# Performance work log

Measured on AMD Instinct MI355X. Metric: run time of the kernel, lower is better.

Reference implementation:

```python
import jax, jax.numpy as jnp
import numpy as np

M_ZEROS = 15
ZETA_WEIGHT = 0.4
SIGMA = 0.1
# First 15 imaginary parts of nontrivial Riemann zeta zeros (get_zeta_zeros(15))
ZETA_ZEROS = np.array([
    14.134725, 21.022040, 25.010858, 30.424876, 32.935062,
    37.586178, 40.918719, 43.327073, 48.005151, 49.773832,
    52.970321, 56.446248, 59.347044, 60.831779, 65.112544,
], dtype=np.float32)

B, T, I, H = 64, 1024, 512, 512


def setup_inputs() -> dict:
    key = jax.random.key(0)
    k = jax.random.split(key, 6)
    s_ih = 1.0 / np.sqrt(I)
    s_hh = 1.0 / np.sqrt(H)
    x = jax.random.normal(k[0], (B, T, I), dtype=jnp.float32)
    W_ih = jax.random.normal(k[1], (4 * H, I), dtype=jnp.float32) * s_ih
    W_hh = jax.random.normal(k[2], (4 * H, H), dtype=jnp.float32) * s_hh
    b_ih = jax.random.normal(k[3], (4 * H,), dtype=jnp.float32) * s_hh
    b_hh = jax.random.normal(k[4], (4 * H,), dtype=jnp.float32) * s_hh
    gammas = jnp.asarray(ZETA_ZEROS)
    phi_init = np.exp(-SIGMA * np.abs(ZETA_ZEROS))
    log_phi = jnp.asarray(np.log(np.exp(phi_init) - 1 + 1e-6).astype(np.float32))
    return {"x": x, "W_ih": W_ih, "W_hh": W_hh, "b_ih": b_ih,
            "b_hh": b_hh, "log_phi": log_phi, "gammas": gammas}


def _zeta_lstm(x, W_ih, W_hh, b_ih, b_hh, log_phi, gammas):
    Bq, Tq, _ = x.shape
    Hq = W_hh.shape[1]
    # Precompute scalar zeta mixing weight per timestep: w_t = sum(phi * cos(g*t)) / M
    phi = jax.nn.softplus(log_phi)                     # [M]
    t_idx = jnp.arange(Tq, dtype=jnp.float32)          # [T]
    cos_mat = jnp.cos(t_idx[:, None] * gammas[None, :])  # [T, M]
    w_ts = (cos_mat @ phi) / M_ZEROS                   # [T]
    # Hoist the input projection out of the scan: [B,T,4H]
    x_proj = jnp.einsum('bti,gi->btg', x, W_ih) + b_ih + b_hh

    def step(carry, inp):
        h, c = carry
        xp_t, w_t = inp
        gates = xp_t + h @ W_hh.T                      # [B, 4H]
        ig, fg, gg, og = jnp.split(gates, 4, axis=-1)
        c_new = jax.nn.sigmoid(fg) * c + jax.nn.sigmoid(ig) * jnp.tanh(gg)
        h_new = jax.nn.sigmoid(og) * jnp.tanh(c_new)
        # zeta memory uses the PREVIOUS h
        h_out = h_new + ZETA_WEIGHT * (w_t * h)
        return (h_out, c_new), h_out

    h0 = jnp.zeros((Bq, Hq), dtype=x.dtype)
    c0 = jnp.zeros((Bq, Hq), dtype=x.dtype)
    xs = (jnp.transpose(x_proj, (1, 0, 2)), w_ts)
    (h_f, c_f), outs = jax.lax.scan(step, (h0, c0), xs)
    outputs = jnp.transpose(outs, (1, 0, 2))           # [B, T, H]
    return outputs, h_f[None, :, :], c_f[None, :, :]


def reference(x, W_ih, W_hh, b_ih, b_hh, log_phi, gammas):
    return _zeta_lstm(x, W_ih, W_hh, b_ih, b_hh, log_phi, gammas)
```

## Files before the change

kernel.cpp:

```cpp
#include <hip/hip_runtime.h>

#define BDIM 64
#define TDIM 1024
#define IDIM 512
#define HDIM 512
#define G4   2048
#define DSLAB 8
#define SLAB_ELEMS (BDIM * HDIM)
#define GROUP_ELEMS (16 * HDIM)

typedef unsigned short u16;
typedef unsigned int u32;
typedef unsigned long long u64;
typedef __attribute__((ext_vector_type(8))) short short8;
typedef __attribute__((ext_vector_type(4))) float f32x4;

__device__ __forceinline__ u16 f2bf(float f) {
    union { float f; unsigned u; } v; v.f = f;
    unsigned u = v.u;
    return (u16)((u + 0x7fffu + ((u >> 16) & 1u)) >> 16);
}
__device__ __forceinline__ float bf2f(u16 h) {
    union { unsigned u; float f; } v; v.u = ((unsigned)h) << 16;
    return v.f;
}
__device__ __forceinline__ float fsig(float x) {
    float e = __builtin_amdgcn_exp2f(x * -1.4426950408889634f);
    return __builtin_amdgcn_rcpf(1.0f + e);
}
__device__ __forceinline__ float ftanh(float x) {
    float e = __builtin_amdgcn_exp2f(x * -2.8853900817779268f);
    return 2.0f * __builtin_amdgcn_rcpf(1.0f + e) - 1.0f;
}

__global__ void prep_kernel(const float* __restrict__ Whh,
                            const float* __restrict__ bih,
                            const float* __restrict__ bhh,
                            const float* __restrict__ log_phi,
                            const float* __restrict__ gammas,
                            u16* __restrict__ whh_bf,
                            float* __restrict__ bias,
                            float* __restrict__ wfull,
                            u32* __restrict__ hbuf32) {
    int idx = blockIdx.x * 256 + threadIdx.x;
    if (idx < G4 * HDIM) whh_bf[idx] = f2bf(Whh[idx]);
    if (idx < G4) bias[idx] = bih[idx] + bhh[idx];
    if (idx < DSLAB * (SLAB_ELEMS / 2))
        hbuf32[idx] = (idx < (SLAB_ELEMS / 2)) ? 0u : 0xffffffffu;
    if (idx < TDIM) {
        float acc = 0.0f;
        #pragma unroll
        for (int m = 0; m < 15; ++m) {
            float lp = log_phi[m];
            float sp = (lp > 15.0f) ? lp : log1pf(expf(lp));
            acc += sp * cosf((float)idx * gammas[m]);
        }
        wfull[idx] = 0.4f * acc / 15.0f;
    }
}

__global__ __launch_bounds__(256) void xproj_gemm(
        const float* __restrict__ X, const float* __restrict__ Wih,
        const float* __restrict__ bias, u16* __restrict__ xproj) {
    const int tid  = threadIdx.x;
    const int m0   = blockIdx.x * 128;
    const int n0   = blockIdx.y * 128;
    const int lane = tid & 63, w = tid >> 6;
    const int l16  = lane & 15, lhi = lane >> 4;
    const int wr   = w >> 1, wc = w & 1;

    __shared__ u16 As[128 * 64];
    __shared__ u16 Bs[128 * 64];

    f32x4 acc[4][4];
    #pragma unroll
    for (int i = 0; i < 4; ++i)
        #pragma unroll
        for (int j = 0; j < 4; ++j) acc[i][j] = (f32x4){0.f, 0.f, 0.f, 0.f};

    for (int kt = 0; kt < 8; ++kt) {
        const int k0 = kt * 64;
        __syncthreads();
        #pragma unroll
        for (int p = 0; p < 4; ++p) {
            int g = p * 256 + tid;
            int row = g >> 3, oct = g & 7;
            const float* src = X + (size_t)(m0 + row) * IDIM + k0 + oct * 8;
            float4 v0 = *(const float4*)src;
            float4 v1 = *(const float4*)(src + 4);
            short8 u;
            u[0] = (short)f2bf(v0.x); u[1] = (short)f2bf(v0.y);
            u[2] = (short)f2bf(v0.z); u[3] = (short)f2bf(v0.w);
            u[4] = (short)f2bf(v1.x); u[5] = (short)f2bf(v1.y);
            u[6] = (short)f2bf(v1.z); u[7] = (short)f2bf(v1.w);
            int so = (oct ^ (row & 7)) * 8;
            *(short8*)&As[row * 64 + so] = u;
        }
        #pragma unroll
        for (int p = 0; p < 4; ++p) {
            int g = p * 256 + tid;
            int row = g >> 3, oct = g & 7;
            const float* src = Wih + (size_t)(n0 + row) * IDIM + k0 + oct * 8;
            float4 v0 = *(const float4*)src;
            float4 v1 = *(const float4*)(src + 4);
            short8 u;
            u[0] = (short)f2bf(v0.x); u[1] = (short)f2bf(v0.y);
            u[2] = (short)f2bf(v0.z); u[3] = (short)f2bf(v0.w);
            u[4] = (short)f2bf(v1.x); u[5] = (short)f2bf(v1.y);
            u[6] = (short)f2bf(v1.z); u[7] = (short)f2bf(v1.w);
            int so = (oct ^ (row & 7)) * 8;
            *(short8*)&Bs[row * 64 + so] = u;
        }
        __syncthreads();
        #pragma unroll
        for (int ks = 0; ks < 2; ++ks) {
            short8 a[4], b[4];
            #pragma unroll
            for (int ai = 0; ai < 4; ++ai) {
                int row = 64 * wr + 16 * ai + l16;
                int oct = (4 * ks + lhi) ^ (row & 7);
                a[ai] = *(const short8*)&As[row * 64 + oct * 8];
            }
            #pragma unroll
            for (int bi = 0; bi < 4; ++bi) {
                int row = 64 * wc + 16 * bi + l16;
                int oct = (4 * ks + lhi) ^ (row & 7);
                b[bi] = *(const short8*)&Bs[row * 64 + oct * 8];
            }
            #pragma unroll
            for (int ai = 0; ai < 4; ++ai)
                #pragma unroll
                for (int bi = 0; bi < 4; ++bi)
                    acc[ai][bi] = __builtin_amdgcn_mfma_f32_16x16x32_bf16(
                        a[ai], b[bi], acc[ai][bi], 0, 0, 0);
        }
    }
    float bv[4];
    #pragma unroll
    for (int bi = 0; bi < 4; ++bi) bv[bi] = bias[n0 + 64 * wc + 16 * bi + l16];
    #pragma unroll
    for (int ai = 0; ai < 4; ++ai) {
        int grow_base = m0 + 64 * wr + 16 * ai + 4 * lhi;
        #pragma unroll
        for (int bi = 0; bi < 4; ++bi) {
            int gcol = n0 + 64 * wc + 16 * bi + l16;
            #pragma unroll
            for (int r = 0; r < 4; ++r) {
                int grow = grow_base + r;
                int b = grow >> 10;
                int t = grow & 1023;
                xproj[((size_t)t * BDIM + b) * G4 + gcol] =
                    f2bf(acc[ai][bi][r] + bv[bi]);
            }
        }
    }
}

__global__ __launch_bounds__(256, 1) void scan_kernel(
        const u16* __restrict__ whh_bf, const float* __restrict__ wfull,
        const u16* __restrict__ xproj, u16* __restrict__ hbuf,
        float* __restrict__ out) {
    const int tid = threadIdx.x;
    const int blk = blockIdx.x;
    const int bg  = blk >> 4;
    const int cgp = blk & 15;
    const int b0  = bg * 16;
    const int c0  = cgp * 32;
    const int lane = tid & 63, w = tid >> 6;
    const int l16 = lane & 15, lhi = lane >> 4;

    __shared__ u16  hfrag[16 * 64 * 8];
    __shared__ float gates[16 * 128];
    __shared__ float wt_s[TDIM];

    for (int i = tid; i < TDIM; i += 256) wt_s[i] = wfull[i];

    short8 Bf0[16], Bf1[16];
    #pragma unroll
    for (int ks = 0; ks < 16; ++ks) {
        int row0 = w * HDIM + c0 + l16;
        int row1 = w * HDIM + c0 + 16 + l16;
        Bf0[ks] = *(const short8*)&whh_bf[(size_t)row0 * HDIM + ks * 32 + lhi * 8];
        Bf1[ks] = *(const short8*)&whh_bf[(size_t)row1 * HDIM + ks * 32 + lhi * 8];
    }

    const int eb = tid >> 4;
    const int j0 = 2 * (tid & 15);
    const int gcol = c0 + j0;
    const int ln_e = eb + 16 * (j0 >> 3);
    const size_t eidx = ((size_t)cgp * 64 + ln_e) * 8 + (j0 & 7);
    float creg0 = 0.f, creg1 = 0.f;
    float hp0 = 0.f, hp1 = 0.f;

    u32 xq0, xq1, xq2, xq3;
    {
        const u16* xb = xproj + (size_t)(b0 + eb) * G4 + gcol;
        xq0 = *(const u32*)(xb + 0 * HDIM);
        xq1 = *(const u32*)(xb + 1 * HDIM);
        xq2 = *(const u32*)(xb + 2 * HDIM);
        xq3 = *(const u32*)(xb + 3 * HDIM);
    }
    __syncthreads();

    for (int t = 0; t < TDIM; ++t) {
        const u16* hsrc = hbuf + (size_t)(t & 7) * SLAB_ELEMS
                               + (size_t)bg * GROUP_ELEMS;

        union F { u64 q[2]; short8 s; } A4[4];
        for (;;) {
            u32 bad = 0;
            #pragma unroll
            for (int i = 0; i < 4; ++i) {
                const int ks = 4 * w + i;
                const u64* p = (const u64*)(hsrc + ks * 512 + lane * 8);
                u64 lo = __hip_atomic_load(p, __ATOMIC_RELAXED, __HIP_MEMORY_SCOPE_AGENT);
                u64 hi = __hip_atomic_load(p + 1, __ATOMIC_RELAXED, __HIP_MEMORY_SCOPE_AGENT);
                A4[i].q[0] = lo; A4[i].q[1] = hi;
                bad |= ((u32)lo == 0xffffffffu) | ((u32)(lo >> 32) == 0xffffffffu) |
                       ((u32)hi == 0xffffffffu) | ((u32)(hi >> 32) == 0xffffffffu);
            }
            if (!__any((int)bad)) break;
        }

        if (t > 0) {
            *(float2*)(out + ((size_t)(b0 + eb) * TDIM + (t - 1)) * HDIM + gcol) =
                make_float2(hp0, hp1);
        }
        u32 nx0 = 0, nx1 = 0, nx2 = 0, nx3 = 0;
        if (t + 1 < TDIM) {
            const u16* xb = xproj + (size_t)(t + 1) * BDIM * G4 +
                            (size_t)(b0 + eb) * G4 + gcol;
            nx0 = *(const u32*)(xb + 0 * HDIM);
            nx1 = *(const u32*)(xb + 1 * HDIM);
            nx2 = *(const u32*)(xb + 2 * HDIM);
            nx3 = *(const u32*)(xb + 3 * HDIM);
        }

        #pragma unroll
        for (int i = 0; i < 4; ++i) {
            const int ks = 4 * w + i;
            *(short8*)&hfrag[(ks * 64 + lane) * 8] = A4[i].s;
        }
        __syncthreads();
        if (t > 0) {
            __hip_atomic_store(
                (u32*)(hbuf + (size_t)((t - 1) & 7) * SLAB_ELEMS +
                       (size_t)bg * GROUP_ELEMS + eidx), 0xffffffffu,
                __ATOMIC_RELAXED, __HIP_MEMORY_SCOPE_AGENT);
        }

        f32x4 acc0 = {0.f, 0.f, 0.f, 0.f}, acc1 = {0.f, 0.f, 0.f, 0.f};
        #pragma unroll
        for (int ks = 0; ks < 16; ++ks) {
            short8 a = *(const short8*)&hfrag[(ks * 64 + lane) * 8];
            acc0 = __builtin_amdgcn_mfma_f32_16x16x32_bf16(a, Bf0[ks], acc0, 0, 0, 0);
            acc1 = __builtin_amdgcn_mfma_f32_16x16x32_bf16(a, Bf1[ks], acc1, 0, 0, 0);
        }
        #pragma unroll
        for (int r = 0; r < 4; ++r) {
            gates[(4 * lhi + r) * 128 + w * 32 + l16]      = acc0[r];
            gates[(4 * lhi + r) * 128 + w * 32 + 16 + l16] = acc1[r];
        }
        __syncthreads();

        const float wt = wt_s[t];
        float x0 = bf2f((u16)(xq0 & 0xffff)), x1 = bf2f((u16)(xq0 >> 16));
        float f0 = bf2f((u16)(xq1 & 0xffff)), f1 = bf2f((u16)(xq1 >> 16));
        float g0 = bf2f((u16)(xq2 & 0xffff)), g1 = bf2f((u16)(xq2 >> 16));
        float o0 = bf2f((u16)(xq3 & 0xffff)), o1 = bf2f((u16)(xq3 >> 16));

        float gi0 = gates[eb * 128 + 0 * 32 + j0]     + x0;
        float gi1 = gates[eb * 128 + 0 * 32 + j0 + 1] + x1;
        float gf0 = gates[eb * 128 + 1 * 32 + j0]     + f0;
        float gf1 = gates[eb * 128 + 1 * 32 + j0 + 1] + f1;
        float gg0 = gates[eb * 128 + 2 * 32 + j0]     + g0;
        float gg1 = gates[eb * 128 + 2 * 32 + j0 + 1] + g1;
        float go0 = gates[eb * 128 + 3 * 32 + j0]     + o0;
        float go1 = gates[eb * 128 + 3 * 32 + j0 + 1] + o1;

        float cn0 = fsig(gf0) * creg0 + fsig(gi0) * ftanh(gg0);
        float cn1 = fsig(gf1) * creg1 + fsig(gi1) * ftanh(gg1);
        float ho0 = fsig(go0) * ftanh(cn0) + wt * hp0;
        float ho1 = fsig(go1) * ftanh(cn1) + wt * hp1;
        creg0 = cn0; creg1 = cn1;
        hp0 = ho0; hp1 = ho1;

        u32 hw = (u32)f2bf(ho0) | ((u32)f2bf(ho1) << 16);
        __hip_atomic_store(
            (u32*)(hbuf + (size_t)((t + 1) & 7) * SLAB_ELEMS +
                   (size_t)bg * GROUP_ELEMS + eidx), hw,
            __ATOMIC_RELAXED, __HIP_MEMORY_SCOPE_AGENT);

        xq0 = nx0; xq1 = nx1; xq2 = nx2; xq3 = nx3;
    }

    *(float2*)(out + ((size_t)(b0 + eb) * TDIM + (TDIM - 1)) * HDIM + gcol) =
        make_float2(hp0, hp1);
    size_t base = (size_t)BDIM * TDIM * HDIM;
    *(float2*)(out + base + (size_t)(b0 + eb) * HDIM + gcol) =
        make_float2(hp0, hp1);
    *(float2*)(out + base + (size_t)BDIM * HDIM + (size_t)(b0 + eb) * HDIM + gcol) =
        make_float2(creg0, creg1);
}

extern "C" void kernel_launch(void* const* d_in, const int* in_sizes, int n_in,
                              void* d_out, int out_size, void* d_ws, size_t ws_size,
                              hipStream_t stream) {
    const float* x       = (const float*)d_in[0];
    const float* Wih     = (const float*)d_in[1];
    const float* Whh     = (const float*)d_in[2];
    const float* bih     = (const float*)d_in[3];
    const float* bhh     = (const float*)d_in[4];
    const float* log_phi = (const float*)d_in[5];
    const float* gammas  = (const float*)d_in[6];
    float* out = (float*)d_out;

    char* ws = (char*)d_ws;
    u16*   whh_bf = (u16*)(ws);
    float* bias   = (float*)(ws + (2u << 20));
    float* wfull  = (float*)(ws + (2u << 20) + 8192);
    u16*   hbuf   = (u16*)(ws + (3u << 20));
    u16*   xproj  = (u16*)(ws + (4u << 20));

    prep_kernel<<<dim3(4096), dim3(256), 0, stream>>>(
        Whh, bih, bhh, log_phi, gammas, whh_bf, bias, wfull, (u32*)hbuf);

    xproj_gemm<<<dim3(512, 16), dim3(256), 0, stream>>>(x, Wih, bias, xproj);

    scan_kernel<<<dim3(64), dim3(256), 0, stream>>>(
        whh_bf, wfull, xproj, hbuf, out);
}
```

Measured before the change: 2.722 ms.

## Pre-convert GEMM inputs to bf16, overlap own-slice MFMAs, add spin sleep

Adds a separate conversion pass that turns x and W_ih into bf16 once, so the input-projection GEMM stops re-converting fp32 tiles every time a block loads them. The bf16 path only runs when the workspace is large enough. In the scan loop, each wave now runs the MFMAs for its own h slice from registers before the block barrier, and it splits the accumulators into two chains to shorten dependency stalls. An s_sleep is added in the spin-wait to cut polling pressure. The costs are an extra full pass over x in memory and possibly higher wake-up latency in the scan.

```diff
diff --git a/kernel.cpp b/kernel.cpp
--- a/kernel.cpp
+++ b/kernel.cpp
@@ -59,6 +59,106 @@
     }
 }
 
+__global__ void cvt_kernel(const float* __restrict__ X, u16* __restrict__ Xbf,
+                           const float* __restrict__ W, u16* __restrict__ Wbf) {
+    const size_t NX8 = (size_t)BDIM * TDIM * IDIM / 8;
+    const size_t NW8 = (size_t)G4 * IDIM / 8;
+    size_t g = (size_t)blockIdx.x * 256 + threadIdx.x;
+    const float* src; u16* dst; size_t off;
+    if (g < NX8) { src = X; dst = Xbf; off = g * 8; }
+    else if (g < NX8 + NW8) { src = W; dst = Wbf; off = (g - NX8) * 8; }
+    else return;
+    float4 v0 = *(const float4*)(src + off);
+    float4 v1 = *(const float4*)(src + off + 4);
+    short8 u;
+    u[0] = (short)f2bf(v0.x); u[1] = (short)f2bf(v0.y);
+    u[2] = (short)f2bf(v0.z); u[3] = (short)f2bf(v0.w);
+    u[4] = (short)f2bf(v1.x); u[5] = (short)f2bf(v1.y);
+    u[6] = (short)f2bf(v1.z); u[7] = (short)f2bf(v1.w);
+    *(short8*)(dst + off) = u;
+}
+
+__global__ __launch_bounds__(256) void xproj_gemm_bf16(
+        const u16* __restrict__ Xbf, const u16* __restrict__ Wihbf,
+        const float* __restrict__ bias, u16* __restrict__ xproj) {
+    const int tid  = threadIdx.x;
+    const int m0   = blockIdx.x * 128;
+    const int n0   = blockIdx.y * 128;
+    const int lane = tid & 63, w = tid >> 6;
+    const int l16  = lane & 15, lhi = lane >> 4;
+    const int wr   = w >> 1, wc = w & 1;
+
+    __shared__ u16 As[128 * 64];
+    __shared__ u16 Bs[128 * 64];
+
+    f32x4 acc[4][4];
+    #pragma unroll
+    for (int i = 0; i < 4; ++i)
+        #pragma unroll
+        for (int j = 0; j < 4; ++j) acc[i][j] = (f32x4){0.f, 0.f, 0.f, 0.f};
+
+    for (int kt = 0; kt < 8; ++kt) {
+        const int k0 = kt * 64;
+        __syncthreads();
+        #pragma unroll
+        for (int p = 0; p < 4; ++p) {
+            int g = p * 256 + tid;
+            int row = g >> 3, oct = g & 7;
+            short8 u = *(const short8*)(Xbf + (size_t)(m0 + row) * IDIM + k0 + oct * 8);
+            *(short8*)&As[row * 64 + ((oct ^ (row & 7)) * 8)] = u;
+        }
+        #pragma unroll
+        for (int p = 0; p < 4; ++p) {
+            int g = p * 256 + tid;
+            int row = g >> 3, oct = g & 7;
+            short8 u = *(const short8*)(Wihbf + (size_t)(n0 + row) * IDIM + k0 + oct * 8);
+            *(short8*)&Bs[row * 64 + ((oct ^ (row & 7)) * 8)] = u;
+        }
+        __syncthreads();
+        #pragma unroll
+        for (int ks = 0; ks < 2; ++ks) {
+            short8 a[4], b[4];
+            #pragma unroll
+            for (int ai = 0; ai < 4; ++ai) {
+                int row = 64 * wr + 16 * ai + l16;
+                int oct = (4 * ks + lhi) ^ (row & 7);
+                a[ai] = *(const short8*)&As[row * 64 + oct * 8];
+            }
+            #pragma unroll
+            for (int bi = 0; bi < 4; ++bi) {
+                int row = 64 * wc + 16 * bi + l16;
+                int oct = (4 * ks + lhi) ^ (row & 7);
+                b[bi] = *(const short8*)&Bs[row * 64 + oct * 8];
+            }
+            #pragma unroll
+            for (int ai = 0; ai < 4; ++ai)
+                #pragma unroll
+                for (int bi = 0; bi < 4; ++bi)
+                    acc[ai][bi] = __builtin_amdgcn_mfma_f32_16x16x32_bf16(
+                        a[ai], b[bi], acc[ai][bi], 0, 0, 0);
+        }
+    }
+    float bv[4];
+    #pragma unroll
+    for (int bi = 0; bi < 4; ++bi) bv[bi] = bias[n0 + 64 * wc + 16 * bi + l16];
+    #pragma unroll
+    for (int ai = 0; ai < 4; ++ai) {
+        int grow_base = m0 + 64 * wr + 16 * ai + 4 * lhi;
+        #pragma unroll
+        for (int bi = 0; bi < 4; ++bi) {
+            int gcol = n0 + 64 * wc + 16 * bi + l16;
+            #pragma unroll
+            for (int r = 0; r < 4; ++r) {
+                int grow = grow_base + r;
+                int b = grow >> 10;
+                int t = grow & 1023;
+                xproj[((size_t)t * BDIM + b) * G4 + gcol] =
+                    f2bf(acc[ai][bi][r] + bv[bi]);
+            }
+        }
+    }
+}
+
 __global__ __launch_bounds__(256) void xproj_gemm(
         const float* __restrict__ X, const float* __restrict__ Wih,
         const float* __restrict__ bias, u16* __restrict__ xproj) {
@@ -93,8 +193,7 @@
             u[2] = (short)f2bf(v0.z); u[3] = (short)f2bf(v0.w);
             u[4] = (short)f2bf(v1.x); u[5] = (short)f2bf(v1.y);
             u[6] = (short)f2bf(v1.z); u[7] = (short)f2bf(v1.w);
-            int so = (oct ^ (row & 7)) * 8;
-            *(short8*)&As[row * 64 + so] = u;
+            *(short8*)&As[row * 64 + ((oct ^ (row & 7)) * 8)] = u;
         }
         #pragma unroll
         for (int p = 0; p < 4; ++p) {
@@ -108,8 +207,7 @@
             u[2] = (short)f2bf(v0.z); u[3] = (short)f2bf(v0.w);
             u[4] = (short)f2bf(v1.x); u[5] = (short)f2bf(v1.y);
             u[6] = (short)f2bf(v1.z); u[7] = (short)f2bf(v1.w);
-            int so = (oct ^ (row & 7)) * 8;
-            *(short8*)&Bs[row * 64 + so] = u;
+            *(short8*)&Bs[row * 64 + ((oct ^ (row & 7)) * 8)] = u;
         }
         __syncthreads();
         #pragma unroll
@@ -220,6 +318,7 @@
                        ((u32)hi == 0xffffffffu) | ((u32)(hi >> 32) == 0xffffffffu);
             }
             if (!__any((int)bad)) break;
+            __builtin_amdgcn_s_sleep(1);
         }
 
         if (t > 0) {
@@ -241,6 +340,26 @@
             const int ks = 4 * w + i;
             *(short8*)&hfrag[(ks * 64 + lane) * 8] = A4[i].s;
         }
+
+        f32x4 acc0a = {0.f, 0.f, 0.f, 0.f}, acc0b = {0.f, 0.f, 0.f, 0.f};
+        f32x4 acc1a = {0.f, 0.f, 0.f, 0.f}, acc1b = {0.f, 0.f, 0.f, 0.f};
+        #define OWN_MFMA(W)                                                               \
+            acc0a = __builtin_amdgcn_mfma_f32_16x16x32_bf16(A4[0].s, Bf0[4*W+0], acc0a, 0, 0, 0); \
+            acc1a = __builtin_amdgcn_mfma_f32_16x16x32_bf16(A4[0].s, Bf1[4*W+0], acc1a, 0, 0, 0); \
+            acc0b = __builtin_amdgcn_mfma_f32_16x16x32_bf16(A4[1].s, Bf0[4*W+1], acc0b, 0, 0, 0); \
+            acc1b = __builtin_amdgcn_mfma_f32_16x16x32_bf16(A4[1].s, Bf1[4*W+1], acc1b, 0, 0, 0); \
+            acc0a = __builtin_amdgcn_mfma_f32_16x16x32_bf16(A4[2].s, Bf0[4*W+2], acc0a, 0, 0, 0); \
+            acc1a = __builtin_amdgcn_mfma_f32_16x16x32_bf16(A4[2].s, Bf1[4*W+2], acc1a, 0, 0, 0); \
+            acc0b = __builtin_amdgcn_mfma_f32_16x16x32_bf16(A4[3].s, Bf0[4*W+3], acc0b, 0, 0, 0); \
+            acc1b = __builtin_amdgcn_mfma_f32_16x16x32_bf16(A4[3].s, Bf1[4*W+3], acc1b, 0, 0, 0);
+        switch (w) {
+            case 0: { OWN_MFMA(0) } break;
+            case 1: { OWN_MFMA(1) } break;
+            case 2: { OWN_MFMA(2) } break;
+            default:{ OWN_MFMA(3) } break;
+        }
+        #undef OWN_MFMA
+
         __syncthreads();
         if (t > 0) {
             __hip_atomic_store(
@@ -249,13 +368,20 @@
                 __ATOMIC_RELAXED, __HIP_MEMORY_SCOPE_AGENT);
         }
 
-        f32x4 acc0 = {0.f, 0.f, 0.f, 0.f}, acc1 = {0.f, 0.f, 0.f, 0.f};
         #pragma unroll
         for (int ks = 0; ks < 16; ++ks) {
+            if ((ks >> 2) == w) continue;
             short8 a = *(const short8*)&hfrag[(ks * 64 + lane) * 8];
-            acc0 = __builtin_amdgcn_mfma_f32_16x16x32_bf16(a, Bf0[ks], acc0, 0, 0, 0);
-            acc1 = __builtin_amdgcn_mfma_f32_16x16x32_bf16(a, Bf1[ks], acc1, 0, 0, 0);
-        }
+            if (ks & 1) {
+                acc0b = __builtin_amdgcn_mfma_f32_16x16x32_bf16(a, Bf0[ks], acc0b, 0, 0, 0);
+                acc1b = __builtin_amdgcn_mfma_f32_16x16x32_bf16(a, Bf1[ks], acc1b, 0, 0, 0);
+            } else {
+                acc0a = __builtin_amdgcn_mfma_f32_16x16x32_bf16(a, Bf0[ks], acc0a, 0, 0, 0);
+                acc1a = __builtin_amdgcn_mfma_f32_16x16x32_bf16(a, Bf1[ks], acc1a, 0, 0, 0);
+            }
+        }
+        f32x4 acc0 = acc0a + acc0b;
+        f32x4 acc1 = acc1a + acc1b;
         #pragma unroll
         for (int r = 0; r < 4; ++r) {
             gates[(4 * lhi + r) * 128 + w * 32 + l16]      = acc0[r];
@@ -321,11 +447,20 @@
     float* wfull  = (float*)(ws + (2u << 20) + 8192);
     u16*   hbuf   = (u16*)(ws + (3u << 20));
     u16*   xproj  = (u16*)(ws + (4u << 20));
+    u16*   x_bf   = (u16*)(ws + (260ull << 20));
+    u16*   wih_bf = (u16*)(ws + (324ull << 20));
+    const bool bf16path = ws_size >= (326ull << 20);
 
     prep_kernel<<<dim3(4096), dim3(256), 0, stream>>>(
         Whh, bih, bhh, log_phi, gammas, whh_bf, bias, wfull, (u32*)hbuf);
 
-    xproj_gemm<<<dim3(512, 16), dim3(256), 0, stream>>>(x, Wih, bias, xproj);
+    if (bf16path) {
+        cvt_kernel<<<dim3(16896), dim3(256), 0, stream>>>(x, x_bf, Wih, wih_bf);
+        xproj_gemm_bf16<<<dim3(512, 16), dim3(256), 0, stream>>>(
+            x_bf, wih_bf, bias, xproj);
+    } else {
+        xproj_gemm<<<dim3(512, 16), dim3(256), 0, stream>>>(x, Wih, bias, xproj);
+    }
 
     scan_kernel<<<dim3(64), dim3(256), 0, stream>>>(
         whh_bf, wfull, xproj, hbuf, out);
```

Result: slower. 2.926 ms (+7.5%).
